# Kernel optimization log

Hardware: AMD Instinct MI355X
Metric: run time of the kernel (lower is better)

The kernel has to match this reference:

```python
import jax, jax.numpy as jnp
import numpy as np

N = 50000            # problem dimension (free subspace)
K = 64               # low-rank dimension of the Hessian model
M = 64               # number of active equality constraints (rows of A)
MAX_CG_ITER = 40     # static bound on CG iterations -> reorth buffer size
CG_TOL = 1e-6
CG_REG = 1e-8
TOL_ABS = 1e-14      # _HRSTCG_TOL_ABS


def setup_inputs() -> dict:
    key = jax.random.key(0)
    k1, k2, k3, k4 = jax.random.split(key, 4)
    g_eff = jax.random.normal(k1, (N,), jnp.float32)
    # SPD diagonal part of the working Hessian: entries in [1, 2)
    diag = jax.random.uniform(k2, (N,), jnp.float32) + 1.0
    # low-rank factor, scaled so U U^T has O(1) spectrum
    U = jax.random.normal(k3, (N, K), jnp.float32) / np.float32(np.sqrt(N))
    # active constraint matrix, scaled so A A^T is well conditioned
    A = jax.random.normal(k4, (M, N), jnp.float32) / np.float32(np.sqrt(N))
    return {"g_eff": g_eff, "diag": diag, "U": U, "A": A}


def _hr_stcg(g_eff, diag, U, A):
    n = g_eff.shape[0]
    dtype = g_eff.dtype
    # exact null-space projector W(v) = v - A^T (A A^T)^{-1} A v
    AAt = A @ A.T + 1e-8 * jnp.eye(A.shape[0], dtype=A.dtype)
    AAt_inv = jnp.linalg.inv(AAt)
    project = lambda v: v - A.T @ (AAt_inv @ (A @ v))
    # working-subspace HVP: H v = diag*v + U (U^T v)  (SPD)
    hvp_work = lambda v: diag * v + U @ (U.T @ v)

    indices = jnp.arange(MAX_CG_ITER)

    Wg = project(g_eff)
    r0 = -Wg
    proj_grad_norm = jnp.sqrt(jnp.maximum(jnp.dot(r0, r0), 0.0))
    rz0 = jnp.dot(r0, r0)  # z0 = r0

    # state: (t, r, z, p, rz, P, HP, pHp_diag, iteration, converged)
    init_state = (
        jnp.zeros(n, dtype), r0, r0, r0, rz0,
        jnp.zeros((MAX_CG_ITER, n), dtype),
        jnp.zeros((MAX_CG_ITER, n), dtype),
        jnp.zeros(MAX_CG_ITER, dtype),
        jnp.array(0),
        jnp.reshape(proj_grad_norm <= TOL_ABS, ()),
    )

    def do_step(s):
        t, r, z, p, rz, P, HP, pHp_diag, it, conv = s
        Hp = hvp_work(p)
        pHp = jnp.dot(p, Hp)
        pp = jnp.dot(p, p)
        abs_floor = CG_REG * proj_grad_norm * proj_grad_norm
        bad_curvature = pHp <= jnp.maximum(CG_REG * pp, abs_floor)
        rp = jnp.dot(r, p)
        stagnation = jnp.abs(rp) < 1e-30
        sc = bad_curvature | stagnation  # short_circuit
        pHp_safe = jnp.maximum(pHp, 1e-30)
        alpha = jnp.where(sc, jnp.asarray(0.0, dtype), rz / pHp_safe)
        t_new = t + alpha * p
        r_new = r - alpha * Hp                 # modified residual recurrence
        z_new = project(r_new)
        P_buf = P.at[it].set(p)
        HP_buf = HP.at[it].set(Hp)
        pHp_buf = pHp_diag.at[it].set(pHp)
        mask_j = indices <= it
        Hz_dots = HP_buf @ z_new               # full H-conjugacy reorth
        pHp_diag_safe = jnp.where(jnp.abs(pHp_buf) > 1e-30, pHp_buf, 1e-30)
        coeffs = jnp.where(mask_j, Hz_dots / pHp_diag_safe, 0.0)
        p_new = z_new - coeffs @ P_buf
        rz_new = jnp.dot(r_new, z_new)
        z_norm = jnp.sqrt(jnp.maximum(jnp.dot(z_new, z_new), 0.0))
        tol_target = jnp.maximum(TOL_ABS, CG_TOL * proj_grad_norm)
        conv_new = (z_norm <= tol_target) | sc
        return (
            jnp.where(sc, t, t_new), jnp.where(sc, r, r_new),
            jnp.where(sc, z, z_new), jnp.where(sc, p, p_new),
            jnp.where(sc, rz, rz_new),
            P_buf, HP_buf, pHp_buf, it + 1, conv_new,
        )

    def step_fn(_i, s):
        return jax.lax.cond(jnp.reshape(s[-1], ()), lambda x: x, do_step, s)

    final = jax.lax.fori_loop(0, MAX_CG_ITER, step_fn, init_state)
    return final[0], proj_grad_norm, final[-1]


def reference(g_eff, diag, U, A):
    # returns (t_k, ||r0||, converged) as in _hr_stcg
    return _hr_stcg(g_eff, diag, U, A)
```

## Files before the change

kernel.cpp:

```cpp
#include <hip/hip_runtime.h>
#include <hip/hip_cooperative_groups.h>
#include <math.h>

namespace cg = cooperative_groups;

#define N_ 50000
#define K_ 64
#define M_ 64
#define MAXIT 40
#define NC 782
#define BSZ 256

#define CG_TOLf  1e-6f
#define CG_REGf  1e-8f
#define TOL_ABSf 1e-14f

#define OFF_Y0   0
#define OFF_PGN2 2048
#define OFF_S0   2080
#define OFF_BAR  2144
#define OFF_AATB 2720
#define OFF_INV  19104
#define OFF_BUFA 23200
#define OFF_BUFB 34016
#define WS_HEAD  38432
#define OFF_PB   38464
#define OFF_HPB  (OFF_PB + MAXIT * N_)

#define BUFA_SZ  5408
#define BUFB_SZ  2208

__device__ __forceinline__ float wred(float v) {
#pragma unroll
  for (int m = 1; m < 64; m <<= 1) v += __shfl_xor(v, m, 64);
  return v;
}

__device__ __forceinline__ float cload(const float* p) {
  return __hip_atomic_load(p, __ATOMIC_RELAXED, __HIP_MEMORY_SCOPE_SYSTEM);
}
__device__ __forceinline__ void cstore(float* p, float v) {
  __hip_atomic_store(p, v, __ATOMIC_RELAXED, __HIP_MEMORY_SCOPE_SYSTEM);
}

__device__ __forceinline__ void gbar(unsigned* bar, int b, int NB, unsigned ep) {
  __syncthreads();
  if (threadIdx.x == 0) {
    const int grp = b & 15;
    const unsigned gsz = (unsigned)((NB - grp + 15) >> 4);
    unsigned o = __hip_atomic_fetch_add(&bar[grp * 32], 1u, __ATOMIC_RELAXED, __HIP_MEMORY_SCOPE_AGENT);
    if (o % gsz == gsz - 1u) {
      unsigned r = __hip_atomic_fetch_add(&bar[16 * 32], 1u, __ATOMIC_RELAXED, __HIP_MEMORY_SCOPE_AGENT);
      if ((r & 15u) == 15u)
        __hip_atomic_fetch_add(&bar[17 * 32], 1u, __ATOMIC_RELAXED, __HIP_MEMORY_SCOPE_AGENT);
    }
    while (__hip_atomic_load(&bar[17 * 32], __ATOMIC_RELAXED, __HIP_MEMORY_SCOPE_SYSTEM) < ep)
      __builtin_amdgcn_s_sleep(2);
  }
  __syncthreads();
}

template<int NK>
__device__ __forceinline__ void consume(const float* buf, int nl, float* dst, int t) {
  const int nq = nl * 16;
  const double* bd = (const double*)buf;
  double xd[NK];
#pragma unroll
  for (int k = 0; k < NK; ++k) {
    int q = t + (k << 8);
    q = (q < nq) ? q : (nq - 1);
    xd[k] = __hip_atomic_load(bd + q, __ATOMIC_RELAXED, __HIP_MEMORY_SCOPE_SYSTEM);
  }
#pragma unroll
  for (int k = 0; k < NK; ++k) {
    const int q = t + (k << 8);
    float2 f;
    __builtin_memcpy(&f, &xd[k], 8);
    float v = f.x + f.y;
    v += __shfl_xor(v, 1, 64);
    v += __shfl_xor(v, 2, 64);
    v += __shfl_xor(v, 4, 64);
    v += __shfl_xor(v, 8, 64);
    if (q < nq && (t & 15) == 0) dst[q >> 4] = v;
  }
}

__global__ __launch_bounds__(BSZ, 4)
void stcg_kernel(const float* __restrict__ g, const float* __restrict__ dg,
                 const float* __restrict__ U, const float* __restrict__ A,
                 float* __restrict__ out, float* __restrict__ ws)
{
  cg::grid_group grid = cg::this_grid();
  const int b = blockIdx.x, NB = gridDim.x, t = threadIdx.x;
  const int wv = t >> 6, lane = t & 63;
  const int base1 = b * 64;
  const int col1 = base1 + lane;
  const bool valid1 = col1 < N_;
  const bool own2 = (b + NB) < NC;
  const int base2 = (b + NB) * 64;
  const int col2 = base2 + lane;
  const bool valid2 = own2 && (col2 < N_);
  const int nv2 = own2 ? min(64, N_ - base2) : 0;
  const int bank = b & 31;

  __shared__ float Als[64 * 65];
  __shared__ float AHPl[41 * 65];
  __shared__ float partA[BSZ];
  __shared__ float rL[64], hpL[64], pL[64];
  __shared__ float rL2[64], hpL2[64], pL2[64];
  __shared__ float ssh[64], cshL[64];
  __shared__ float rowk[64], fsh[64];
  __shared__ float redL[184];
  __shared__ float pHpdL[MAXIT];

  float* Pb  = ws + OFF_PB;
  float* HPb = ws + OFF_HPB;
  unsigned* bar = (unsigned*)(ws + OFF_BAR);
  unsigned ep = 0;

  float t_ = 0.f, r_ = 0.f, p_ = 0.f, d_ = 0.f;
  float t2_ = 0.f, r2_ = 0.f, p2_ = 0.f, d2_ = 0.f;
  float invr[16];
  float ur[16];
  if (wv == 0 && valid1) d_ = dg[col1];
  if (wv == 1 && valid2) d2_ = dg[col2];

  for (int idx = b * BSZ + t; idx < WS_HEAD; idx += NB * BSZ) ws[idx] = 0.f;
  grid.sync();

  float aat[4][4];
#pragma unroll
  for (int a = 0; a < 4; ++a)
#pragma unroll
    for (int c = 0; c < 4; ++c) aat[a][c] = 0.f;
  const int tr4 = (t >> 4) << 2, tc4 = (t & 15) << 2;

  if (wv == 0) cshL[lane] = valid1 ? g[col1] : 0.f;
#pragma unroll
  for (int kk = 0; kk < 16; ++kk) {
    const int m = wv * 16 + kk;
    Als[m * 65 + lane] = valid1 ? A[(size_t)m * N_ + col1] : 0.f;
  }
  __syncthreads();
  {
#pragma unroll 4
    for (int j = 0; j < 64; ++j) {
      float a0 = Als[(tr4 + 0) * 65 + j], a1 = Als[(tr4 + 1) * 65 + j];
      float a2 = Als[(tr4 + 2) * 65 + j], a3 = Als[(tr4 + 3) * 65 + j];
      float b0 = Als[(tc4 + 0) * 65 + j], b1 = Als[(tc4 + 1) * 65 + j];
      float b2 = Als[(tc4 + 2) * 65 + j], b3 = Als[(tc4 + 3) * 65 + j];
      aat[0][0] += a0 * b0; aat[0][1] += a0 * b1; aat[0][2] += a0 * b2; aat[0][3] += a0 * b3;
      aat[1][0] += a1 * b0; aat[1][1] += a1 * b1; aat[1][2] += a1 * b2; aat[1][3] += a1 * b3;
      aat[2][0] += a2 * b0; aat[2][1] += a2 * b1; aat[2][2] += a2 * b2; aat[2][3] += a2 * b3;
      aat[3][0] += a3 * b0; aat[3][1] += a3 * b1; aat[3][2] += a3 * b2; aat[3][3] += a3 * b3;
    }
    if (wv == 0) {
      float s = 0.f;
#pragma unroll 8
      for (int c = 0; c < 64; ++c) s += Als[lane * 65 + c] * cshL[c];
      atomicAdd(&ws[OFF_Y0 + lane * 32 + bank], s);
    }
  }
  if (own2) {
    __syncthreads();
    if (wv == 1) cshL[lane] = valid2 ? g[col2] : 0.f;
#pragma unroll
    for (int kk = 0; kk < 16; ++kk) {
      const int m = wv * 16 + kk;
      Als[m * 65 + lane] = valid2 ? A[(size_t)m * N_ + col2] : 0.f;
    }
    __syncthreads();
#pragma unroll 4
    for (int j = 0; j < 64; ++j) {
      float a0 = Als[(tr4 + 0) * 65 + j], a1 = Als[(tr4 + 1) * 65 + j];
      float a2 = Als[(tr4 + 2) * 65 + j], a3 = Als[(tr4 + 3) * 65 + j];
      float b0 = Als[(tc4 + 0) * 65 + j], b1 = Als[(tc4 + 1) * 65 + j];
      float b2 = Als[(tc4 + 2) * 65 + j], b3 = Als[(tc4 + 3) * 65 + j];
      aat[0][0] += a0 * b0; aat[0][1] += a0 * b1; aat[0][2] += a0 * b2; aat[0][3] += a0 * b3;
      aat[1][0] += a1 * b0; aat[1][1] += a1 * b1; aat[1][2] += a1 * b2; aat[1][3] += a1 * b3;
      aat[2][0] += a2 * b0; aat[2][1] += a2 * b1; aat[2][2] += a2 * b2; aat[2][3] += a2 * b3;
      aat[3][0] += a3 * b0; aat[3][1] += a3 * b1; aat[3][2] += a3 * b2; aat[3][3] += a3 * b3;
    }
    if (wv == 1) {
      float s = 0.f;
#pragma unroll 8
      for (int c = 0; c < 64; ++c) s += Als[lane * 65 + c] * cshL[c];
      atomicAdd(&ws[OFF_Y0 + lane * 32 + bank], s);
    }
    __syncthreads();
#pragma unroll
    for (int kk = 0; kk < 16; ++kk) {
      const int m = wv * 16 + kk;
      Als[m * 65 + lane] = valid1 ? A[(size_t)m * N_ + col1] : 0.f;
    }
  }
  {
    float* bk4 = ws + OFF_AATB + (b & 3) * 4096;
#pragma unroll
    for (int a = 0; a < 4; ++a)
#pragma unroll
      for (int c = 0; c < 4; ++c)
        atomicAdd(&bk4[(tr4 + a) * 64 + (tc4 + c)], aat[a][c]);
  }
  gbar(bar, b, NB, ++ep);

  if (b == 0) {
#pragma unroll
    for (int kk = 0; kk < 16; ++kk) {
      const int idx = lane * 64 + wv * 16 + kk;
      float v = cload(&ws[OFF_AATB + idx]) + cload(&ws[OFF_AATB + 4096 + idx]) +
                cload(&ws[OFF_AATB + 8192 + idx]) + cload(&ws[OFF_AATB + 12288 + idx]);
      invr[kk] = v + ((lane == wv * 16 + kk) ? 1e-8f : 0.f);
    }
    __syncthreads();
    for (int k = 0; k < 64; ++k) {
      if (lane == k) {
#pragma unroll
        for (int kk = 0; kk < 16; ++kk) rowk[wv * 16 + kk] = invr[kk];
      }
      if (wv == (k >> 4)) fsh[lane] = invr[k & 15];
      __syncthreads();
      const float piv = 1.0f / rowk[k];
      const float fr = fsh[lane];
#pragma unroll
      for (int kk = 0; kk < 16; ++kk) {
        const int c = wv * 16 + kk;
        const float rkc = rowk[c] * piv;
        float v;
        if (lane == k) v = (c == k) ? piv : rkc;
        else           v = (c == k) ? (-fr * piv) : (invr[kk] - fr * rkc);
        invr[kk] = v;
      }
      __syncthreads();
    }
#pragma unroll
    for (int kk = 0; kk < 16; ++kk)
      cstore(&ws[OFF_INV + lane * 64 + wv * 16 + kk], invr[kk]);
    if (t < 64) {
      float a = 0.f;
#pragma unroll
      for (int k2 = 0; k2 < 32; ++k2) a += cload(&ws[OFF_Y0 + t * 32 + k2]);
      redL[t] = a;
    }
    __syncthreads();
    {
      float ps = 0.f;
#pragma unroll
      for (int kk = 0; kk < 16; ++kk) ps += invr[kk] * redL[wv * 16 + kk];
      partA[t] = ps;
    }
    __syncthreads();
    if (t < 64) cstore(&ws[OFF_S0 + t], partA[t] + partA[64 + t] + partA[128 + t] + partA[192 + t]);
  }
  {
    if (valid1) {
      const float4* Up = reinterpret_cast<const float4*>(U + (size_t)col1 * K_ + wv * 16);
      float4 u0 = Up[0], u1 = Up[1], u2 = Up[2], u3 = Up[3];
      ur[0]=u0.x; ur[1]=u0.y; ur[2]=u0.z; ur[3]=u0.w;
      ur[4]=u1.x; ur[5]=u1.y; ur[6]=u1.z; ur[7]=u1.w;
      ur[8]=u2.x; ur[9]=u2.y; ur[10]=u2.z; ur[11]=u2.w;
      ur[12]=u3.x; ur[13]=u3.y; ur[14]=u3.z; ur[15]=u3.w;
    } else {
#pragma unroll
      for (int kk = 0; kk < 16; ++kk) ur[kk] = 0.f;
    }
  }
  gbar(bar, b, NB, ++ep);

  if (b != 0) {
#pragma unroll
    for (int kk = 0; kk < 16; ++kk)
      invr[kk] = cload(&ws[OFF_INV + lane * 64 + wv * 16 + kk]);
  }

  if (t < 64) ssh[t] = cload(&ws[OFF_S0 + t]);
  __syncthreads();
  {
    float* B0 = ws + OFF_BUFB;
    if (wv == 0) {
      float acc = 0.f;
#pragma unroll 8
      for (int m = 0; m < 64; ++m) acc += Als[m * 65 + lane] * ssh[m];
      float r0 = valid1 ? (acc - g[col1]) : 0.f;
      r_ = r0; p_ = r0; pL[lane] = r0;
      const float v  = wred(r0 * r0);
      const float v0 = wred(d_ * r0 * r0);
      if (lane == 0) {
        atomicAdd(&B0[(64 + 0) * 32 + bank], v0);
        atomicAdd(&B0[(64 + 1) * 32 + bank], v);
        atomicAdd(&B0[(64 + 2) * 32 + bank], v);
        atomicAdd(&B0[(64 + 3) * 32 + bank], v);
        atomicAdd(&B0[(64 + 4) * 32 + bank], v);
        atomicAdd(&ws[OFF_PGN2 + bank], v);
      }
    }
    if (wv == 1 && own2) {
      float acc = 0.f;
      if (valid2) {
#pragma unroll 8
        for (int m = 0; m < 64; ++m) acc += A[(size_t)m * N_ + col2] * ssh[m];
      }
      float r0 = valid2 ? (acc - g[col2]) : 0.f;
      r2_ = r0; p2_ = r0; pL2[lane] = r0;
      const float v  = wred(r0 * r0);
      const float v0 = wred(d2_ * r0 * r0);
      if (lane == 0) {
        atomicAdd(&B0[(64 + 0) * 32 + bank], v0);
        atomicAdd(&B0[(64 + 1) * 32 + bank], v);
        atomicAdd(&B0[(64 + 2) * 32 + bank], v);
        atomicAdd(&B0[(64 + 3) * 32 + bank], v);
        atomicAdd(&B0[(64 + 4) * 32 + bank], v);
        atomicAdd(&ws[OFF_PGN2 + bank], v);
      }
    }
    __syncthreads();
#pragma unroll
    for (int kk = 0; kk < 16; ++kk) {
      const float s = wred(ur[kk] * pL[lane]);
      if (lane == 0) atomicAdd(&B0[(wv * 16 + kk) * 32 + bank], s);
    }
    if (wv == 1 && own2) {
      float s = 0.f;
      for (int c = 0; c < nv2; ++c) s += U[(size_t)(base2 + c) * K_ + lane] * pL2[c];
      atomicAdd(&B0[lane * 32 + bank], s);
    }
  }
  gbar(bar, b, NB, ++ep);

  float pgn2v = 0.f;
#pragma unroll
  for (int k = 0; k < 32; ++k) pgn2v += cload(&ws[OFF_PGN2 + k]);
  const float pgn = sqrtf(fmaxf(pgn2v, 0.f));
  const float tolv = fmaxf(TOL_ABSf, CG_TOLf * pgn);
  bool sc_r = false, convf = false;

  for (int it = 0;; ++it) {
    const int p = it & 1;
    float* BB  = ws + OFF_BUFB + p * BUFB_SZ;
    float* BBn = ws + OFF_BUFB + (p ^ 1) * BUFB_SZ;
    float* BA  = ws + OFF_BUFA + p * BUFA_SZ;
    float* BAn = ws + OFF_BUFA + (p ^ 1) * BUFA_SZ;

    consume<5>(BB, 69, redL, t);
    for (int u = b * BSZ + t; u < BUFB_SZ; u += NB * BSZ) cstore(&BBn[u], 0.f);
    __syncthreads();
    const float pDp = redL[64], pp = redL[65], rp = redL[66], rz = redL[67], zz = redL[68];
    convf = sc_r || (sqrtf(fmaxf(zz, 0.f)) <= tolv);
    if (convf || it == MAXIT) break;

    const float ww = wred(redL[lane] * redL[lane]);
    const float pHp = pDp + ww;
    const bool bad = pHp <= fmaxf(CG_REGf * pp, CG_REGf * pgn2v);
    sc_r = bad || (fabsf(rp) < 1e-30f);
    const float alpha = sc_r ? 0.f : rz / fmaxf(pHp, 1e-30f);
    if (t == 0) pHpdL[it] = pHp;

    {
      float acc = 0.f;
#pragma unroll
      for (int kk = 0; kk < 16; ++kk) acc += ur[kk] * redL[wv * 16 + kk];
      partA[t] = acc;
    }
    __syncthreads();
    if (wv == 0) {
      const float hp = d_ * p_ + partA[lane] + partA[64 + lane] + partA[128 + lane] + partA[192 + lane];
      t_ += alpha * p_;
      r_ -= alpha * hp;
      if (valid1) { Pb[(size_t)it * N_ + col1] = p_; HPb[(size_t)it * N_ + col1] = hp; }
      rL[lane] = r_; hpL[lane] = hp;
    }
    if (wv == 1 && own2) {
      float hp = d2_ * p2_;
      if (valid2) {
        const float4* Urow = reinterpret_cast<const float4*>(U + (size_t)col2 * K_);
#pragma unroll
        for (int k4 = 0; k4 < 16; ++k4) {
          float4 u = Urow[k4];
          hp += u.x * redL[4 * k4 + 0] + u.y * redL[4 * k4 + 1] + u.z * redL[4 * k4 + 2] + u.w * redL[4 * k4 + 3];
        }
      }
      t2_ += alpha * p2_;
      r2_ -= alpha * hp;
      if (valid2) { Pb[(size_t)it * N_ + col2] = p2_; HPb[(size_t)it * N_ + col2] = hp; }
      rL2[lane] = r2_; hpL2[lane] = hp;
    }
    __syncthreads();
    if (wv == 0) {
      float sy = 0.f, sa = 0.f;
#pragma unroll 8
      for (int c = 0; c < 64; ++c) {
        const float av = Als[lane * 65 + c];
        sy += av * rL[c];
        sa += av * hpL[c];
      }
      atomicAdd(&BA[lane * 32 + bank], sy);
      atomicAdd(&BA[(64 + lane) * 32 + bank], sa);
    } else if (wv == 1 && own2) {
      float sy = 0.f, sa = 0.f;
      for (int c = 0; c < nv2; ++c) {
        const float av = A[(size_t)lane * N_ + base2 + c];
        sy += av * rL2[c];
        sa += av * hpL2[c];
      }
      atomicAdd(&BA[lane * 32 + bank], sy);
      atomicAdd(&BA[(64 + lane) * 32 + bank], sa);
    }
    {
      const int hw0 = own2 ? 2 : 1;
      if (wv >= hw0) {
        const int nhw = 4 - hw0;
        for (int j = wv - hw0; j <= it; j += nhw) {
          float s = ((j == it) ? hpL[lane] : (valid1 ? HPb[(size_t)j * N_ + col1] : 0.f)) * rL[lane];
          if (own2) {
            const float hv2 = (j == it) ? hpL2[lane] : (valid2 ? HPb[(size_t)j * N_ + col2] : 0.f);
            s += hv2 * rL2[lane];
          }
          s = wred(s);
          if (lane == 0) atomicAdd(&BA[(128 + j) * 32 + bank], s);
        }
      }
    }
    gbar(bar, b, NB, ++ep);

    consume<11>(BA, 129 + it, redL, t);
    for (int u = b * BSZ + t; u < BUFA_SZ; u += NB * BSZ) cstore(&BAn[u], 0.f);
    __syncthreads();
    if (t < 64) AHPl[it * 65 + t] = redL[64 + t];
    {
      float ps = 0.f;
#pragma unroll
      for (int kk = 0; kk < 16; ++kk) ps += invr[kk] * redL[wv * 16 + kk];
      partA[t] = ps;
    }
    __syncthreads();
    if (t < 64) ssh[t] = partA[t] + partA[64 + t] + partA[128 + t] + partA[192 + t];
    __syncthreads();
    if (t < 64) {
      float c = 0.f;
      if (t <= it) {
        float hz = redL[128 + t];
        const float* ar = AHPl + t * 65;
#pragma unroll 8
        for (int m = 0; m < 64; ++m) hz -= ar[m] * ssh[m];
        const float den = pHpdL[t];
        c = hz / ((fabsf(den) > 1e-30f) ? den : 1e-30f);
      }
      cshL[t] = c;
    }
    __syncthreads();
    {
      float accA = 0.f;
#pragma unroll
      for (int kk = 0; kk < 16; ++kk) {
        const int m = wv * 16 + kk;
        accA += Als[m * 65 + lane] * ssh[m];
      }
      partA[t] = accA;
    }
    __syncthreads();
    if (wv == 0) {
      float z = r_ - (partA[lane] + partA[64 + lane] + partA[128 + lane] + partA[192 + lane]);
      if (!valid1) z = 0.f;
      hpL[lane] = z;
    }
    if (wv == 1 && own2) {
      float acc = 0.f;
      if (valid2) {
#pragma unroll 8
        for (int m = 0; m < 64; ++m) acc += A[(size_t)m * N_ + col2] * ssh[m];
      }
      hpL2[lane] = valid2 ? (r2_ - acc) : 0.f;
    }
    __syncthreads();
    {
      float accP = 0.f;
      if (valid1) {
        for (int j = wv; j <= it; j += 4) accP += cshL[j] * Pb[(size_t)j * N_ + col1];
      }
      partA[t] = accP;
    }
    __syncthreads();
    if (wv == 0) {
      const float z = hpL[lane];
      float pn = z - (partA[lane] + partA[64 + lane] + partA[128 + lane] + partA[192 + lane]);
      if (!valid1) pn = 0.f;
      p_ = pn; pL[lane] = pn;
      const float v0 = wred(d_ * pn * pn);
      const float v1 = wred(pn * pn);
      const float v2 = wred(r_ * pn);
      const float v3 = wred(r_ * z);
      const float v4 = wred(z * z);
      if (lane == 0) {
        atomicAdd(&BBn[(64 + 0) * 32 + bank], v0);
        atomicAdd(&BBn[(64 + 1) * 32 + bank], v1);
        atomicAdd(&BBn[(64 + 2) * 32 + bank], v2);
        atomicAdd(&BBn[(64 + 3) * 32 + bank], v3);
        atomicAdd(&BBn[(64 + 4) * 32 + bank], v4);
      }
    }
    if (wv == 1 && own2) {
      const float z2 = hpL2[lane];
      float accP2 = 0.f;
      if (valid2) {
        for (int j = 0; j <= it; ++j) accP2 += cshL[j] * Pb[(size_t)j * N_ + col2];
      }
      float pn = valid2 ? (z2 - accP2) : 0.f;
      p2_ = pn; pL2[lane] = pn;
      const float v0 = wred(d2_ * pn * pn);
      const float v1 = wred(pn * pn);
      const float v2 = wred(r2_ * pn);
      const float v3 = wred(r2_ * z2);
      const float v4 = wred(z2 * z2);
      if (lane == 0) {
        atomicAdd(&BBn[(64 + 0) * 32 + bank], v0);
        atomicAdd(&BBn[(64 + 1) * 32 + bank], v1);
        atomicAdd(&BBn[(64 + 2) * 32 + bank], v2);
        atomicAdd(&BBn[(64 + 3) * 32 + bank], v3);
        atomicAdd(&BBn[(64 + 4) * 32 + bank], v4);
      }
    }
    __syncthreads();
#pragma unroll
    for (int kk = 0; kk < 16; ++kk) {
      const float s = wred(ur[kk] * pL[lane]);
      if (lane == 0) atomicAdd(&BBn[(wv * 16 + kk) * 32 + bank], s);
    }
    if (wv == 1 && own2) {
      float s = 0.f;
      for (int c = 0; c < nv2; ++c) s += U[(size_t)(base2 + c) * K_ + lane] * pL2[c];
      atomicAdd(&BBn[lane * 32 + bank], s);
    }
    gbar(bar, b, NB, ++ep);
  }

  if (wv == 0 && valid1) out[col1] = t_;
  if (wv == 1 && valid2) out[col2] = t2_;
  if (b == 0 && t == 0) {
    out[N_]     = pgn;
    out[N_ + 1] = convf ? 1.f : 0.f;
  }
}

extern "C" void kernel_launch(void* const* d_in, const int* in_sizes, int n_in,
                              void* d_out, int out_size, void* d_ws, size_t ws_size,
                              hipStream_t stream) {
  (void)in_sizes; (void)n_in; (void)out_size; (void)ws_size;
  const float* g  = (const float*)d_in[0];
  const float* dg = (const float*)d_in[1];
  const float* U  = (const float*)d_in[2];
  const float* A  = (const float*)d_in[3];
  float* out = (float*)d_out;
  float* ws  = (float*)d_ws;

  int dev = 0;
  hipGetDevice(&dev);
  int nCU = 0;
  hipDeviceGetAttribute(&nCU, hipDeviceAttributeMultiprocessorCount, dev);
  if (nCU <= 0) nCU = 256;
  int maxB = 0;
  hipOccupancyMaxActiveBlocksPerMultiprocessor(&maxB, stcg_kernel, BSZ, 0);
  if (maxB <= 0) maxB = 1;
  int nblk = maxB * nCU;
  if (nblk > NC) nblk = NC;
  if (nblk < 391) nblk = 391;

  void* args[] = {(void*)&g, (void*)&dg, (void*)&U, (void*)&A, (void*)&out, (void*)&ws};
  hipLaunchCooperativeKernel(stcg_kernel, dim3(nblk), dim3(BSZ), args, 0, stream);
}
```

Baseline: 623.9 us.

## Halve grid barriers per CG iteration via precomputed Gram matrices and triple-buffered reductions

Precomputes the A·U and U^T·U Gram matrices once, then updates the projected residual and the A·Hp and U^T·Hp quantities algebraically from reduced small vectors. This lets each CG iteration run with a single grid barrier instead of two. Reductions rotate across three buffers so that zeroing the next buffer does not race with the current one. In exchange it adds a setup phase with extra global atomics, stores D·Hp instead of Hp, and carries more reduction lines, and the recurrence-based updates may drift numerically.

```diff
diff --git a/kernel.cpp b/kernel.cpp
--- a/kernel.cpp
+++ b/kernel.cpp
@@ -6,7 +6,6 @@
 
 #define N_ 50000
 #define K_ 64
-#define M_ 64
 #define MAXIT 40
 #define NC 782
 #define BSZ 256
@@ -15,20 +14,26 @@
 #define CG_REGf  1e-8f
 #define TOL_ABSf 1e-14f
 
-#define OFF_Y0   0
-#define OFF_PGN2 2048
-#define OFF_S0   2080
-#define OFF_BAR  2144
-#define OFF_AATB 2720
-#define OFF_INV  19104
-#define OFF_BUFA 23200
-#define OFF_BUFB 34016
-#define WS_HEAD  38432
-#define OFF_PB   38464
-#define OFF_HPB  (OFF_PB + MAXIT * N_)
-
-#define BUFA_SZ  5408
-#define BUFB_SZ  2208
+#define L_W    8
+#define L_V    72
+#define L_UDP  136
+#define L_Q    200
+#define NLINES 264
+#define BUF_SZ (NLINES * 32)
+
+#define OFF_PGN2 0
+#define OFF_BAR  32
+#define OFF_AATB 608
+#define OFF_GB   16992
+#define OFF_SB   33376
+#define OFF_INV  49760
+#define OFF_S0   53856
+#define OFF_YG   53920
+#define OFF_BUF  55968
+#define WS_HEAD  81312
+#define OFF_AHPG 81312
+#define OFF_PB   (OFF_AHPG + NC * MAXIT * 64)
+#define OFF_DHPB (OFF_PB + MAXIT * N_)
 
 __device__ __forceinline__ float wred(float v) {
 #pragma unroll
@@ -93,46 +98,61 @@
   cg::grid_group grid = cg::this_grid();
   const int b = blockIdx.x, NB = gridDim.x, t = threadIdx.x;
   const int wv = t >> 6, lane = t & 63;
-  const int base1 = b * 64;
-  const int col1 = base1 + lane;
+  const int base1 = b * 64, col1 = base1 + lane;
   const bool valid1 = col1 < N_;
   const bool own2 = (b + NB) < NC;
-  const int base2 = (b + NB) * 64;
-  const int col2 = base2 + lane;
+  const int base2 = (b + NB) * 64, col2 = base2 + lane;
   const bool valid2 = own2 && (col2 < N_);
   const int nv2 = own2 ? min(64, N_ - base2) : 0;
   const int bank = b & 31;
 
   __shared__ float Als[64 * 65];
-  __shared__ float AHPl[41 * 65];
-  __shared__ float partA[BSZ];
-  __shared__ float rL[64], hpL[64], pL[64];
-  __shared__ float rL2[64], hpL2[64], pL2[64];
-  __shared__ float ssh[64], cshL[64];
+  __shared__ float uhpL[41 * 65];
+  __shared__ float partA[BSZ], partB[BSZ];
+  __shared__ float redL[NLINES];
+  __shared__ float yL[64], urL[64], ssh[64], cshL[64];
+  __shared__ float pL[64], dpL[64];
+  __shared__ float pL2[64], dp2L[64];
+  __shared__ float ucL[64];
   __shared__ float rowk[64], fsh[64];
-  __shared__ float redL[184];
-  __shared__ float pHpdL[MAXIT];
-
-  float* Pb  = ws + OFF_PB;
-  float* HPb = ws + OFF_HPB;
+  __shared__ float hrL[MAXIT + 1], pHpdL[MAXIT + 1];
+
+  float* Pb   = ws + OFF_PB;
+  float* DHPb = ws + OFF_DHPB;
+  float* ahpG = ws + OFF_AHPG + (size_t)b * (MAXIT * 64);
   unsigned* bar = (unsigned*)(ws + OFF_BAR);
   unsigned ep = 0;
 
   float t_ = 0.f, r_ = 0.f, p_ = 0.f, d_ = 0.f;
   float t2_ = 0.f, r2_ = 0.f, p2_ = 0.f, d2_ = 0.f;
-  float invr[16];
-  float ur[16];
-  if (wv == 0 && valid1) d_ = dg[col1];
+  float invr[16], Sr[16], Gr[16], ur[16];
+
+  d_ = valid1 ? dg[col1] : 0.f;
   if (wv == 1 && valid2) d2_ = dg[col2];
+
+  if (valid1) {
+    const float4* Up = reinterpret_cast<const float4*>(U + (size_t)col1 * K_ + wv * 16);
+    float4 u0 = Up[0], u1 = Up[1], u2 = Up[2], u3 = Up[3];
+    ur[0]=u0.x; ur[1]=u0.y; ur[2]=u0.z; ur[3]=u0.w;
+    ur[4]=u1.x; ur[5]=u1.y; ur[6]=u1.z; ur[7]=u1.w;
+    ur[8]=u2.x; ur[9]=u2.y; ur[10]=u2.z; ur[11]=u2.w;
+    ur[12]=u3.x; ur[13]=u3.y; ur[14]=u3.z; ur[15]=u3.w;
+  } else {
+#pragma unroll
+    for (int kk = 0; kk < 16; ++kk) ur[kk] = 0.f;
+  }
 
   for (int idx = b * BSZ + t; idx < WS_HEAD; idx += NB * BSZ) ws[idx] = 0.f;
   grid.sync();
 
   float aat[4][4];
+  float Gacc[16], Sacc[16];
 #pragma unroll
   for (int a = 0; a < 4; ++a)
 #pragma unroll
     for (int c = 0; c < 4; ++c) aat[a][c] = 0.f;
+#pragma unroll
+  for (int kk = 0; kk < 16; ++kk) { Gacc[kk] = 0.f; Sacc[kk] = 0.f; }
   const int tr4 = (t >> 4) << 2, tc4 = (t & 15) << 2;
 
   if (wv == 0) cshL[lane] = valid1 ? g[col1] : 0.f;
@@ -145,25 +165,41 @@
   {
 #pragma unroll 4
     for (int j = 0; j < 64; ++j) {
-      float a0 = Als[(tr4 + 0) * 65 + j], a1 = Als[(tr4 + 1) * 65 + j];
-      float a2 = Als[(tr4 + 2) * 65 + j], a3 = Als[(tr4 + 3) * 65 + j];
-      float b0 = Als[(tc4 + 0) * 65 + j], b1 = Als[(tc4 + 1) * 65 + j];
-      float b2 = Als[(tc4 + 2) * 65 + j], b3 = Als[(tc4 + 3) * 65 + j];
-      aat[0][0] += a0 * b0; aat[0][1] += a0 * b1; aat[0][2] += a0 * b2; aat[0][3] += a0 * b3;
-      aat[1][0] += a1 * b0; aat[1][1] += a1 * b1; aat[1][2] += a1 * b2; aat[1][3] += a1 * b3;
-      aat[2][0] += a2 * b0; aat[2][1] += a2 * b1; aat[2][2] += a2 * b2; aat[2][3] += a2 * b3;
-      aat[3][0] += a3 * b0; aat[3][1] += a3 * b1; aat[3][2] += a3 * b2; aat[3][3] += a3 * b3;
+      float a0 = Als[(tr4+0)*65+j], a1 = Als[(tr4+1)*65+j];
+      float a2 = Als[(tr4+2)*65+j], a3 = Als[(tr4+3)*65+j];
+      float b0 = Als[(tc4+0)*65+j], b1 = Als[(tc4+1)*65+j];
+      float b2 = Als[(tc4+2)*65+j], b3 = Als[(tc4+3)*65+j];
+      aat[0][0]+=a0*b0; aat[0][1]+=a0*b1; aat[0][2]+=a0*b2; aat[0][3]+=a0*b3;
+      aat[1][0]+=a1*b0; aat[1][1]+=a1*b1; aat[1][2]+=a1*b2; aat[1][3]+=a1*b3;
+      aat[2][0]+=a2*b0; aat[2][1]+=a2*b1; aat[2][2]+=a2*b2; aat[2][3]+=a2*b3;
+      aat[3][0]+=a3*b0; aat[3][1]+=a3*b1; aat[3][2]+=a3*b2; aat[3][3]+=a3*b3;
     }
     if (wv == 0) {
       float s = 0.f;
 #pragma unroll 8
       for (int c = 0; c < 64; ++c) s += Als[lane * 65 + c] * cshL[c];
-      atomicAdd(&ws[OFF_Y0 + lane * 32 + bank], s);
-    }
+      atomicAdd(&ws[OFF_YG + lane * 32 + bank], s);
+    }
+  }
+  for (int c = 0; c < 64; ++c) {
+    if (lane == c) {
+#pragma unroll
+      for (int kk = 0; kk < 16; ++kk) ucL[wv * 16 + kk] = ur[kk];
+    }
+    __syncthreads();
+    const float a = Als[lane * 65 + c];
+    const float uL = ucL[lane];
+#pragma unroll
+    for (int kk = 0; kk < 16; ++kk) {
+      const float u2 = ucL[wv * 16 + kk];
+      Gacc[kk] += a * u2;
+      Sacc[kk] += uL * u2;
+    }
+    __syncthreads();
   }
   if (own2) {
-    __syncthreads();
     if (wv == 1) cshL[lane] = valid2 ? g[col2] : 0.f;
+    __syncthreads();
 #pragma unroll
     for (int kk = 0; kk < 16; ++kk) {
       const int m = wv * 16 + kk;
@@ -172,22 +208,35 @@
     __syncthreads();
 #pragma unroll 4
     for (int j = 0; j < 64; ++j) {
-      float a0 = Als[(tr4 + 0) * 65 + j], a1 = Als[(tr4 + 1) * 65 + j];
-      float a2 = Als[(tr4 + 2) * 65 + j], a3 = Als[(tr4 + 3) * 65 + j];
-      float b0 = Als[(tc4 + 0) * 65 + j], b1 = Als[(tc4 + 1) * 65 + j];
-      float b2 = Als[(tc4 + 2) * 65 + j], b3 = Als[(tc4 + 3) * 65 + j];
-      aat[0][0] += a0 * b0; aat[0][1] += a0 * b1; aat[0][2] += a0 * b2; aat[0][3] += a0 * b3;
-      aat[1][0] += a1 * b0; aat[1][1] += a1 * b1; aat[1][2] += a1 * b2; aat[1][3] += a1 * b3;
-      aat[2][0] += a2 * b0; aat[2][1] += a2 * b1; aat[2][2] += a2 * b2; aat[2][3] += a2 * b3;
-      aat[3][0] += a3 * b0; aat[3][1] += a3 * b1; aat[3][2] += a3 * b2; aat[3][3] += a3 * b3;
+      float a0 = Als[(tr4+0)*65+j], a1 = Als[(tr4+1)*65+j];
+      float a2 = Als[(tr4+2)*65+j], a3 = Als[(tr4+3)*65+j];
+      float b0 = Als[(tc4+0)*65+j], b1 = Als[(tc4+1)*65+j];
+      float b2 = Als[(tc4+2)*65+j], b3 = Als[(tc4+3)*65+j];
+      aat[0][0]+=a0*b0; aat[0][1]+=a0*b1; aat[0][2]+=a0*b2; aat[0][3]+=a0*b3;
+      aat[1][0]+=a1*b0; aat[1][1]+=a1*b1; aat[1][2]+=a1*b2; aat[1][3]+=a1*b3;
+      aat[2][0]+=a2*b0; aat[2][1]+=a2*b1; aat[2][2]+=a2*b2; aat[2][3]+=a2*b3;
+      aat[3][0]+=a3*b0; aat[3][1]+=a3*b1; aat[3][2]+=a3*b2; aat[3][3]+=a3*b3;
     }
     if (wv == 1) {
       float s = 0.f;
 #pragma unroll 8
       for (int c = 0; c < 64; ++c) s += Als[lane * 65 + c] * cshL[c];
-      atomicAdd(&ws[OFF_Y0 + lane * 32 + bank], s);
-    }
-    __syncthreads();
+      atomicAdd(&ws[OFF_YG + lane * 32 + bank], s);
+    }
+    __syncthreads();
+    for (int c = 0; c < 64; ++c) {
+      if (t < 64) ucL[t] = (base2 + c < N_) ? U[(size_t)(base2 + c) * K_ + t] : 0.f;
+      __syncthreads();
+      const float a = Als[lane * 65 + c];
+      const float uL = ucL[lane];
+#pragma unroll
+      for (int kk = 0; kk < 16; ++kk) {
+        const float u2 = ucL[wv * 16 + kk];
+        Gacc[kk] += a * u2;
+        Sacc[kk] += uL * u2;
+      }
+      __syncthreads();
+    }
 #pragma unroll
     for (int kk = 0; kk < 16; ++kk) {
       const int m = wv * 16 + kk;
@@ -201,6 +250,14 @@
 #pragma unroll
       for (int c = 0; c < 4; ++c)
         atomicAdd(&bk4[(tr4 + a) * 64 + (tc4 + c)], aat[a][c]);
+    float* gb = ws + OFF_GB + (b & 3) * 4096;
+    float* sb = ws + OFF_SB + (b & 3) * 4096;
+#pragma unroll
+    for (int kk = 0; kk < 16; ++kk) {
+      const int idx = lane * 64 + wv * 16 + kk;
+      atomicAdd(&gb[idx], Gacc[kk]);
+      atomicAdd(&sb[idx], Sacc[kk]);
+    }
   }
   gbar(bar, b, NB, ++ep);
 
@@ -239,7 +296,7 @@
     if (t < 64) {
       float a = 0.f;
 #pragma unroll
-      for (int k2 = 0; k2 < 32; ++k2) a += cload(&ws[OFF_Y0 + t * 32 + k2]);
+      for (int k2 = 0; k2 < 32; ++k2) a += cload(&ws[OFF_YG + t * 32 + k2]);
       redL[t] = a;
     }
     __syncthreads();
@@ -252,21 +309,15 @@
     __syncthreads();
     if (t < 64) cstore(&ws[OFF_S0 + t], partA[t] + partA[64 + t] + partA[128 + t] + partA[192 + t]);
   }
-  {
-    if (valid1) {
-      const float4* Up = reinterpret_cast<const float4*>(U + (size_t)col1 * K_ + wv * 16);
-      float4 u0 = Up[0], u1 = Up[1], u2 = Up[2], u3 = Up[3];
-      ur[0]=u0.x; ur[1]=u0.y; ur[2]=u0.z; ur[3]=u0.w;
-      ur[4]=u1.x; ur[5]=u1.y; ur[6]=u1.z; ur[7]=u1.w;
-      ur[8]=u2.x; ur[9]=u2.y; ur[10]=u2.z; ur[11]=u2.w;
-      ur[12]=u3.x; ur[13]=u3.y; ur[14]=u3.z; ur[15]=u3.w;
-    } else {
-#pragma unroll
-      for (int kk = 0; kk < 16; ++kk) ur[kk] = 0.f;
-    }
+#pragma unroll
+  for (int kk = 0; kk < 16; ++kk) {
+    const int idx = lane * 64 + wv * 16 + kk;
+    Gr[kk] = cload(&ws[OFF_GB + idx]) + cload(&ws[OFF_GB + 4096 + idx]) +
+             cload(&ws[OFF_GB + 8192 + idx]) + cload(&ws[OFF_GB + 12288 + idx]);
+    Sr[kk] = cload(&ws[OFF_SB + idx]) + cload(&ws[OFF_SB + 4096 + idx]) +
+             cload(&ws[OFF_SB + 8192 + idx]) + cload(&ws[OFF_SB + 12288 + idx]);
   }
   gbar(bar, b, NB, ++ep);
-
   if (b != 0) {
 #pragma unroll
     for (int kk = 0; kk < 16; ++kk)
@@ -275,55 +326,92 @@
 
   if (t < 64) ssh[t] = cload(&ws[OFF_S0 + t]);
   __syncthreads();
-  {
-    float* B0 = ws + OFF_BUFB;
-    if (wv == 0) {
-      float acc = 0.f;
-#pragma unroll 8
-      for (int m = 0; m < 64; ++m) acc += Als[m * 65 + lane] * ssh[m];
-      float r0 = valid1 ? (acc - g[col1]) : 0.f;
-      r_ = r0; p_ = r0; pL[lane] = r0;
-      const float v  = wred(r0 * r0);
-      const float v0 = wred(d_ * r0 * r0);
-      if (lane == 0) {
-        atomicAdd(&B0[(64 + 0) * 32 + bank], v0);
-        atomicAdd(&B0[(64 + 1) * 32 + bank], v);
-        atomicAdd(&B0[(64 + 2) * 32 + bank], v);
-        atomicAdd(&B0[(64 + 3) * 32 + bank], v);
-        atomicAdd(&B0[(64 + 4) * 32 + bank], v);
-        atomicAdd(&ws[OFF_PGN2 + bank], v);
-      }
-    }
-    if (wv == 1 && own2) {
-      float acc = 0.f;
-      if (valid2) {
-#pragma unroll 8
-        for (int m = 0; m < 64; ++m) acc += A[(size_t)m * N_ + col2] * ssh[m];
-      }
-      float r0 = valid2 ? (acc - g[col2]) : 0.f;
-      r2_ = r0; p2_ = r0; pL2[lane] = r0;
-      const float v  = wred(r0 * r0);
-      const float v0 = wred(d2_ * r0 * r0);
-      if (lane == 0) {
-        atomicAdd(&B0[(64 + 0) * 32 + bank], v0);
-        atomicAdd(&B0[(64 + 1) * 32 + bank], v);
-        atomicAdd(&B0[(64 + 2) * 32 + bank], v);
-        atomicAdd(&B0[(64 + 3) * 32 + bank], v);
-        atomicAdd(&B0[(64 + 4) * 32 + bank], v);
-        atomicAdd(&ws[OFF_PGN2 + bank], v);
-      }
-    }
-    __syncthreads();
-#pragma unroll
-    for (int kk = 0; kk < 16; ++kk) {
-      const float s = wred(ur[kk] * pL[lane]);
-      if (lane == 0) atomicAdd(&B0[(wv * 16 + kk) * 32 + bank], s);
-    }
-    if (wv == 1 && own2) {
-      float s = 0.f;
-      for (int c = 0; c < nv2; ++c) s += U[(size_t)(base2 + c) * K_ + lane] * pL2[c];
-      atomicAdd(&B0[lane * 32 + bank], s);
-    }
+  float* B0 = ws + OFF_BUF;
+  if (wv == 0) {
+    float acc = 0.f;
+#pragma unroll 8
+    for (int m = 0; m < 64; ++m) acc += Als[m * 65 + lane] * ssh[m];
+    float r0 = valid1 ? (acc - g[col1]) : 0.f;
+    r_ = r0; p_ = r0; pL[lane] = r0;
+  }
+  if (wv == 1 && own2) {
+    float acc = 0.f;
+    if (valid2) {
+#pragma unroll 8
+      for (int m = 0; m < 64; ++m) acc += A[(size_t)m * N_ + col2] * ssh[m];
+    }
+    float r0 = valid2 ? (acc - g[col2]) : 0.f;
+    r2_ = r0; p2_ = r0; pL2[lane] = r0;
+    dp2L[lane] = d2_ * r0;
+  }
+  __syncthreads();
+  if (wv == 2) dpL[lane] = d_ * pL[lane];
+  __syncthreads();
+  if (wv == 0) {
+    const float rr  = wred(p_ * p_);
+    const float pdp = wred(d_ * p_ * p_);
+    const float pdd = wred(d_ * d_ * p_ * p_);
+    if (lane == 0) {
+      atomicAdd(&B0[0 * 32 + bank], pdp);
+      atomicAdd(&B0[1 * 32 + bank], rr);
+      atomicAdd(&B0[2 * 32 + bank], rr);
+      atomicAdd(&B0[3 * 32 + bank], rr);
+      atomicAdd(&B0[4 * 32 + bank], rr);
+      atomicAdd(&B0[5 * 32 + bank], pdp);
+      atomicAdd(&B0[6 * 32 + bank], pdd);
+      atomicAdd(&ws[OFF_PGN2 + bank], rr);
+    }
+    float sy = 0.f, sv = 0.f;
+#pragma unroll 8
+    for (int c = 0; c < 64; ++c) {
+      const float av = Als[lane * 65 + c];
+      sy += av * pL[c];
+      sv += av * dpL[c];
+    }
+    atomicAdd(&B0[(L_Q + lane) * 32 + bank], sy);
+    atomicAdd(&B0[(L_V + lane) * 32 + bank], sv);
+  }
+  if (wv == 1 && own2) {
+    const float rr  = wred(p2_ * p2_);
+    const float pdp = wred(d2_ * p2_ * p2_);
+    const float pdd = wred(d2_ * d2_ * p2_ * p2_);
+    if (lane == 0) {
+      atomicAdd(&B0[0 * 32 + bank], pdp);
+      atomicAdd(&B0[1 * 32 + bank], rr);
+      atomicAdd(&B0[2 * 32 + bank], rr);
+      atomicAdd(&B0[3 * 32 + bank], rr);
+      atomicAdd(&B0[4 * 32 + bank], rr);
+      atomicAdd(&B0[5 * 32 + bank], pdp);
+      atomicAdd(&B0[6 * 32 + bank], pdd);
+      atomicAdd(&ws[OFF_PGN2 + bank], rr);
+    }
+    float sy = 0.f, sv = 0.f;
+    for (int c = 0; c < nv2; ++c) {
+      const float av = A[(size_t)lane * N_ + base2 + c];
+      sy += av * pL2[c];
+      sv += av * dp2L[c];
+    }
+    atomicAdd(&B0[(L_Q + lane) * 32 + bank], sy);
+    atomicAdd(&B0[(L_V + lane) * 32 + bank], sv);
+  }
+#pragma unroll
+  for (int kk = 0; kk < 16; ++kk) {
+    const float sw = wred(ur[kk] * pL[lane]);
+    const float su = wred(ur[kk] * dpL[lane]);
+    if (lane == 0) {
+      atomicAdd(&B0[(L_W + wv * 16 + kk) * 32 + bank], sw);
+      atomicAdd(&B0[(L_UDP + wv * 16 + kk) * 32 + bank], su);
+    }
+  }
+  if (wv == 1 && own2) {
+    float sw = 0.f, su = 0.f;
+    for (int c = 0; c < nv2; ++c) {
+      const float u = U[(size_t)(base2 + c) * K_ + lane];
+      sw += u * pL2[c];
+      su += u * dp2L[c];
+    }
+    atomicAdd(&B0[(L_W + lane) * 32 + bank], sw);
+    atomicAdd(&B0[(L_UDP + lane) * 32 + bank], su);
   }
   gbar(bar, b, NB, ++ep);
 
@@ -335,200 +423,217 @@
   bool sc_r = false, convf = false;
 
   for (int it = 0;; ++it) {
-    const int p = it & 1;
-    float* BB  = ws + OFF_BUFB + p * BUFB_SZ;
-    float* BBn = ws + OFF_BUFB + (p ^ 1) * BUFB_SZ;
-    float* BA  = ws + OFF_BUFA + p * BUFA_SZ;
-    float* BAn = ws + OFF_BUFA + (p ^ 1) * BUFA_SZ;
-
-    consume<5>(BB, 69, redL, t);
-    for (int u = b * BSZ + t; u < BUFB_SZ; u += NB * BSZ) cstore(&BBn[u], 0.f);
-    __syncthreads();
-    const float pDp = redL[64], pp = redL[65], rp = redL[66], rz = redL[67], zz = redL[68];
+    float* CB  = ws + OFF_BUF + (it % 3) * BUF_SZ;
+    float* PBf = ws + OFF_BUF + ((it + 1) % 3) * BUF_SZ;
+    float* ZB  = ws + OFF_BUF + ((it + 2) % 3) * BUF_SZ;
+    const int nl = (it == 0) ? NLINES : (L_Q + it);
+    consume<17>(CB, nl, redL, t);
+    for (int u = b * BSZ + t; u < BUF_SZ; u += NB * BSZ) cstore(&ZB[u], 0.f);
+    __syncthreads();
+    if (it == 0 && t < 64) { yL[t] = redL[L_Q + t]; urL[t] = redL[L_W + t]; }
+    const float pDp = redL[0], pp = redL[1], rp = redL[2], rz = redL[3];
+    const float zz = redL[4], pdr = redL[5], pdd = redL[6];
     convf = sc_r || (sqrtf(fmaxf(zz, 0.f)) <= tolv);
     if (convf || it == MAXIT) break;
-
-    const float ww = wred(redL[lane] * redL[lane]);
+    __syncthreads();
+
+    const float ww = wred(redL[L_W + lane] * redL[L_W + lane]);
     const float pHp = pDp + ww;
     const bool bad = pHp <= fmaxf(CG_REGf * pp, CG_REGf * pgn2v);
     sc_r = bad || (fabsf(rp) < 1e-30f);
     const float alpha = sc_r ? 0.f : rz / fmaxf(pHp, 1e-30f);
     if (t == 0) pHpdL[it] = pHp;
 
+    const float wur  = wred(redL[L_W + lane] * urL[lane]);
+    const float wudp = wred(redL[L_W + lane] * redL[L_UDP + lane]);
+    const float hpr  = pdr + wur;
+
+    {
+      float sw = 0.f, gw = 0.f;
+#pragma unroll
+      for (int kk = 0; kk < 16; ++kk) {
+        const float wk = redL[L_W + wv * 16 + kk];
+        sw += Sr[kk] * wk;
+        gw += Gr[kk] * wk;
+      }
+      partA[t] = sw; partB[t] = gw;
+    }
+    __syncthreads();
+    if (t < 64) {
+      const float Sw = partA[t] + partA[64 + t] + partA[128 + t] + partA[192 + t];
+      const float Gw = partB[t] + partB[64 + t] + partB[128 + t] + partB[192 + t];
+      const float uh = redL[L_UDP + t] + Sw;
+      const float ah = redL[L_V + t] + Gw;
+      uhpL[it * 65 + t] = uh;
+      ahpG[it * 64 + t] = ah;
+      yL[t]  -= alpha * ah;
+      urL[t] -= alpha * uh;
+    }
+    __syncthreads();
+    const float wuhp = wred(redL[L_W + lane] * uhpL[it * 65 + lane]);
+    const float hpHp_it = pdd + wudp + wuhp;
+    if (t < it) {
+      float q = redL[L_Q + t];
+      const float* uhr = &uhpL[t * 65];
+#pragma unroll 8
+      for (int k = 0; k < 64; ++k) q += uhr[k] * redL[L_W + k];
+      hrL[t] -= alpha * q;
+    } else if (t == it) {
+      hrL[t] = hpr - alpha * hpHp_it;
+    }
+    {
+      float ps = 0.f;
+#pragma unroll
+      for (int kk = 0; kk < 16; ++kk) ps += invr[kk] * yL[wv * 16 + kk];
+      partA[t] = ps;
+    }
+    __syncthreads();
+    if (t < 64) ssh[t] = partA[t] + partA[64 + t] + partA[128 + t] + partA[192 + t];
+    __syncthreads();
+    if (t <= it) {
+      float hz = hrL[t];
+      const float* ar = &ahpG[t * 64];
+#pragma unroll 8
+      for (int m = 0; m < 64; ++m) hz -= ar[m] * ssh[m];
+      const float den = pHpdL[t];
+      cshL[t] = hz / ((fabsf(den) > 1e-30f) ? den : 1e-30f);
+    }
     {
       float acc = 0.f;
 #pragma unroll
-      for (int kk = 0; kk < 16; ++kk) acc += ur[kk] * redL[wv * 16 + kk];
+      for (int kk = 0; kk < 16; ++kk) acc += ur[kk] * redL[L_W + wv * 16 + kk];
       partA[t] = acc;
     }
     __syncthreads();
+    float zv = 0.f, pn = 0.f;
     if (wv == 0) {
       const float hp = d_ * p_ + partA[lane] + partA[64 + lane] + partA[128 + lane] + partA[192 + lane];
       t_ += alpha * p_;
+      if (valid1) { Pb[(size_t)it * N_ + col1] = p_; DHPb[(size_t)it * N_ + col1] = d_ * hp; }
       r_ -= alpha * hp;
-      if (valid1) { Pb[(size_t)it * N_ + col1] = p_; HPb[(size_t)it * N_ + col1] = hp; }
-      rL[lane] = r_; hpL[lane] = hp;
     }
     if (wv == 1 && own2) {
-      float hp = d2_ * p2_;
+      float hp2 = d2_ * p2_;
       if (valid2) {
         const float4* Urow = reinterpret_cast<const float4*>(U + (size_t)col2 * K_);
 #pragma unroll
         for (int k4 = 0; k4 < 16; ++k4) {
           float4 u = Urow[k4];
-          hp += u.x * redL[4 * k4 + 0] + u.y * redL[4 * k4 + 1] + u.z * redL[4 * k4 + 2] + u.w * redL[4 * k4 + 3];
+          hp2 += u.x * redL[L_W + 4*k4] + u.y * redL[L_W + 4*k4+1] +
+                 u.z * redL[L_W + 4*k4+2] + u.w * redL[L_W + 4*k4+3];
         }
       }
       t2_ += alpha * p2_;
-      r2_ -= alpha * hp;
-      if (valid2) { Pb[(size_t)it * N_ + col2] = p2_; HPb[(size_t)it * N_ + col2] = hp; }
-      rL2[lane] = r2_; hpL2[lane] = hp;
+      if (valid2) { Pb[(size_t)it * N_ + col2] = p2_; DHPb[(size_t)it * N_ + col2] = d2_ * hp2; }
+      r2_ -= alpha * hp2;
+    }
+    __syncthreads();
+    {
+      float accA = 0.f;
+#pragma unroll
+      for (int kk = 0; kk < 16; ++kk) {
+        const int m = wv * 16 + kk;
+        accA += Als[m * 65 + lane] * ssh[m];
+      }
+      partA[t] = accA;
+      float accP = 0.f;
+      if (valid1) {
+        for (int j = wv; j <= it; j += 4) accP += cshL[j] * Pb[(size_t)j * N_ + col1];
+      }
+      partB[t] = accP;
     }
     __syncthreads();
     if (wv == 0) {
-      float sy = 0.f, sa = 0.f;
-#pragma unroll 8
-      for (int c = 0; c < 64; ++c) {
-        const float av = Als[lane * 65 + c];
-        sy += av * rL[c];
-        sa += av * hpL[c];
-      }
-      atomicAdd(&BA[lane * 32 + bank], sy);
-      atomicAdd(&BA[(64 + lane) * 32 + bank], sa);
-    } else if (wv == 1 && own2) {
-      float sy = 0.f, sa = 0.f;
+      zv = r_ - (partA[lane] + partA[64 + lane] + partA[128 + lane] + partA[192 + lane]);
+      pn = zv - (partB[lane] + partB[64 + lane] + partB[128 + lane] + partB[192 + lane]);
+      if (!valid1) { zv = 0.f; pn = 0.f; }
+      p_ = pn; pL[lane] = pn;
+    }
+    if (wv == 1 && own2) {
+      float accA2 = 0.f, accP2 = 0.f;
+      if (valid2) {
+#pragma unroll 8
+        for (int m = 0; m < 64; ++m) accA2 += A[(size_t)m * N_ + col2] * ssh[m];
+        for (int j = 0; j <= it; ++j) accP2 += cshL[j] * Pb[(size_t)j * N_ + col2];
+      }
+      float z2 = valid2 ? (r2_ - accA2) : 0.f;
+      float pn2 = valid2 ? (z2 - accP2) : 0.f;
+      p2_ = pn2; pL2[lane] = pn2; dp2L[lane] = d2_ * pn2;
+      const float v0 = wred(d2_ * pn2 * pn2);
+      const float v1 = wred(pn2 * pn2);
+      const float v2 = wred(r2_ * pn2);
+      const float v3 = wred(r2_ * z2);
+      const float v4 = wred(z2 * z2);
+      const float v5 = wred(d2_ * pn2 * r2_);
+      const float v6 = wred(d2_ * d2_ * pn2 * pn2);
+      if (lane == 0) {
+        atomicAdd(&PBf[0 * 32 + bank], v0);
+        atomicAdd(&PBf[1 * 32 + bank], v1);
+        atomicAdd(&PBf[2 * 32 + bank], v2);
+        atomicAdd(&PBf[3 * 32 + bank], v3);
+        atomicAdd(&PBf[4 * 32 + bank], v4);
+        atomicAdd(&PBf[5 * 32 + bank], v5);
+        atomicAdd(&PBf[6 * 32 + bank], v6);
+      }
+    }
+    __syncthreads();
+    if (wv == 2) dpL[lane] = d_ * pL[lane];
+    __syncthreads();
+#pragma unroll
+    for (int kk = 0; kk < 16; ++kk) {
+      const float sw = wred(ur[kk] * pL[lane]);
+      const float su = wred(ur[kk] * dpL[lane]);
+      if (lane == 0) {
+        atomicAdd(&PBf[(L_W + wv * 16 + kk) * 32 + bank], sw);
+        atomicAdd(&PBf[(L_UDP + wv * 16 + kk) * 32 + bank], su);
+      }
+    }
+    if (wv == 0) {
+      const float v0 = wred(d_ * pn * pn);
+      const float v1 = wred(pn * pn);
+      const float v2 = wred(r_ * pn);
+      const float v3 = wred(r_ * zv);
+      const float v4 = wred(zv * zv);
+      const float v5 = wred(d_ * pn * r_);
+      const float v6 = wred(d_ * d_ * pn * pn);
+      if (lane == 0) {
+        atomicAdd(&PBf[0 * 32 + bank], v0);
+        atomicAdd(&PBf[1 * 32 + bank], v1);
+        atomicAdd(&PBf[2 * 32 + bank], v2);
+        atomicAdd(&PBf[3 * 32 + bank], v3);
+        atomicAdd(&PBf[4 * 32 + bank], v4);
+        atomicAdd(&PBf[5 * 32 + bank], v5);
+        atomicAdd(&PBf[6 * 32 + bank], v6);
+      }
+      float sv = 0.f;
+#pragma unroll 8
+      for (int c = 0; c < 64; ++c) sv += Als[lane * 65 + c] * dpL[c];
+      atomicAdd(&PBf[(L_V + lane) * 32 + bank], sv);
+    }
+    if (wv == 1 && own2) {
+      float sv = 0.f;
+      for (int c = 0; c < nv2; ++c) sv += A[(size_t)lane * N_ + base2 + c] * dp2L[c];
+      atomicAdd(&PBf[(L_V + lane) * 32 + bank], sv);
+      float sw = 0.f, su = 0.f;
       for (int c = 0; c < nv2; ++c) {
-        const float av = A[(size_t)lane * N_ + base2 + c];
-        sy += av * rL2[c];
-        sa += av * hpL2[c];
-      }
-      atomicAdd(&BA[lane * 32 + bank], sy);
-      atomicAdd(&BA[(64 + lane) * 32 + bank], sa);
+        const float u = U[(size_t)(base2 + c) * K_ + lane];
+        sw += u * pL2[c];
+        su += u * dp2L[c];
+      }
+      atomicAdd(&PBf[(L_W + lane) * 32 + bank], sw);
+      atomicAdd(&PBf[(L_UDP + lane) * 32 + bank], su);
     }
     {
       const int hw0 = own2 ? 2 : 1;
       if (wv >= hw0) {
         const int nhw = 4 - hw0;
         for (int j = wv - hw0; j <= it; j += nhw) {
-          float s = ((j == it) ? hpL[lane] : (valid1 ? HPb[(size_t)j * N_ + col1] : 0.f)) * rL[lane];
-          if (own2) {
-            const float hv2 = (j == it) ? hpL2[lane] : (valid2 ? HPb[(size_t)j * N_ + col2] : 0.f);
-            s += hv2 * rL2[lane];
-          }
+          float s = (valid1 ? DHPb[(size_t)j * N_ + col1] : 0.f) * pL[lane];
+          if (own2) s += (valid2 ? DHPb[(size_t)j * N_ + col2] : 0.f) * pL2[lane];
           s = wred(s);
-          if (lane == 0) atomicAdd(&BA[(128 + j) * 32 + bank], s);
+          if (lane == 0) atomicAdd(&PBf[(L_Q + j) * 32 + bank], s);
         }
       }
-    }
-    gbar(bar, b, NB, ++ep);
-
-    consume<11>(BA, 129 + it, redL, t);
-    for (int u = b * BSZ + t; u < BUFA_SZ; u += NB * BSZ) cstore(&BAn[u], 0.f);
-    __syncthreads();
-    if (t < 64) AHPl[it * 65 + t] = redL[64 + t];
-    {
-      float ps = 0.f;
-#pragma unroll
-      for (int kk = 0; kk < 16; ++kk) ps += invr[kk] * redL[wv * 16 + kk];
-      partA[t] = ps;
-    }
-    __syncthreads();
-    if (t < 64) ssh[t] = partA[t] + partA[64 + t] + partA[128 + t] + partA[192 + t];
-    __syncthreads();
-    if (t < 64) {
-      float c = 0.f;
-      if (t <= it) {
-        float hz = redL[128 + t];
-        const float* ar = AHPl + t * 65;
-#pragma unroll 8
-        for (int m = 0; m < 64; ++m) hz -= ar[m] * ssh[m];
-        const float den = pHpdL[t];
-        c = hz / ((fabsf(den) > 1e-30f) ? den : 1e-30f);
-      }
-      cshL[t] = c;
-    }
-    __syncthreads();
-    {
-      float accA = 0.f;
-#pragma unroll
-      for (int kk = 0; kk < 16; ++kk) {
-        const int m = wv * 16 + kk;
-        accA += Als[m * 65 + lane] * ssh[m];
-      }
-      partA[t] = accA;
-    }
-    __syncthreads();
-    if (wv == 0) {
-      float z = r_ - (partA[lane] + partA[64 + lane] + partA[128 + lane] + partA[192 + lane]);
-      if (!valid1) z = 0.f;
-      hpL[lane] = z;
-    }
-    if (wv == 1 && own2) {
-      float acc = 0.f;
-      if (valid2) {
-#pragma unroll 8
-        for (int m = 0; m < 64; ++m) acc += A[(size_t)m * N_ + col2] * ssh[m];
-      }
-      hpL2[lane] = valid2 ? (r2_ - acc) : 0.f;
-    }
-    __syncthreads();
-    {
-      float accP = 0.f;
-      if (valid1) {
-        for (int j = wv; j <= it; j += 4) accP += cshL[j] * Pb[(size_t)j * N_ + col1];
-      }
-      partA[t] = accP;
-    }
-    __syncthreads();
-    if (wv == 0) {
-      const float z = hpL[lane];
-      float pn = z - (partA[lane] + partA[64 + lane] + partA[128 + lane] + partA[192 + lane]);
-      if (!valid1) pn = 0.f;
-      p_ = pn; pL[lane] = pn;
-      const float v0 = wred(d_ * pn * pn);
-      const float v1 = wred(pn * pn);
-      const float v2 = wred(r_ * pn);
-      const float v3 = wred(r_ * z);
-      const float v4 = wred(z * z);
-      if (lane == 0) {
-        atomicAdd(&BBn[(64 + 0) * 32 + bank], v0);
-        atomicAdd(&BBn[(64 + 1) * 32 + bank], v1);
-        atomicAdd(&BBn[(64 + 2) * 32 + bank], v2);
-        atomicAdd(&BBn[(64 + 3) * 32 + bank], v3);
-        atomicAdd(&BBn[(64 + 4) * 32 + bank], v4);
-      }
-    }
-    if (wv == 1 && own2) {
-      const float z2 = hpL2[lane];
-      float accP2 = 0.f;
-      if (valid2) {
-        for (int j = 0; j <= it; ++j) accP2 += cshL[j] * Pb[(size_t)j * N_ + col2];
-      }
-      float pn = valid2 ? (z2 - accP2) : 0.f;
-      p2_ = pn; pL2[lane] = pn;
-      const float v0 = wred(d2_ * pn * pn);
-      const float v1 = wred(pn * pn);
-      const float v2 = wred(r2_ * pn);
-      const float v3 = wred(r2_ * z2);
-      const float v4 = wred(z2 * z2);
-      if (lane == 0) {
-        atomicAdd(&BBn[(64 + 0) * 32 + bank], v0);
-        atomicAdd(&BBn[(64 + 1) * 32 + bank], v1);
-        atomicAdd(&BBn[(64 + 2) * 32 + bank], v2);
-        atomicAdd(&BBn[(64 + 3) * 32 + bank], v3);
-        atomicAdd(&BBn[(64 + 4) * 32 + bank], v4);
-      }
-    }
-    __syncthreads();
-#pragma unroll
-    for (int kk = 0; kk < 16; ++kk) {
-      const float s = wred(ur[kk] * pL[lane]);
-      if (lane == 0) atomicAdd(&BBn[(wv * 16 + kk) * 32 + bank], s);
-    }
-    if (wv == 1 && own2) {
-      float s = 0.f;
-      for (int c = 0; c < nv2; ++c) s += U[(size_t)(base2 + c) * K_ + lane] * pL2[c];
-      atomicAdd(&BBn[lane * 32 + bank], s);
     }
     gbar(bar, b, NB, ++ep);
   }
```

Result: slower. 1.061 ms (+70.1%).
